# Performance work log

Measured on AMD Instinct MI355X. Metric: run time of the kernel, lower is better.

## Reference

```python
import jax, jax.numpy as jnp
import numpy as np

N = 50000
E = 800000
D_IN = 128
D_H = 128


def setup_inputs() -> dict:
    key = jax.random.key(0)
    ks = jax.random.split(key, 12)
    x = jax.random.normal(ks[0], (N, D_IN), dtype=jnp.float32)
    edge_index = jax.random.randint(ks[1], (2, E), 0, N, dtype=jnp.int32)
    reranker_scores = jax.random.uniform(ks[2], (N,), dtype=jnp.float32)
    s = 1.0 / np.sqrt(D_IN)
    # SAGEConv layer 1: lin_l (neighbors, with bias), lin_r (root, no bias)
    Wl1 = jax.random.uniform(ks[3], (D_H, D_IN), jnp.float32, -s, s)
    bl1 = jax.random.uniform(ks[4], (D_H,), jnp.float32, -s, s)
    Wr1 = jax.random.uniform(ks[5], (D_H, D_IN), jnp.float32, -s, s)
    # SAGEConv layer 2
    sh = 1.0 / np.sqrt(D_H)
    Wl2 = jax.random.uniform(ks[6], (D_H, D_H), jnp.float32, -sh, sh)
    bl2 = jax.random.uniform(ks[7], (D_H,), jnp.float32, -sh, sh)
    Wr2 = jax.random.uniform(ks[8], (D_H, D_H), jnp.float32, -sh, sh)
    # score head Linear(hidden, 1)
    Ws = jax.random.uniform(ks[9], (1, D_H), jnp.float32, -sh, sh)
    bs = jax.random.uniform(ks[10], (1,), jnp.float32, -sh, sh)
    alpha = jnp.asarray(0.65, dtype=jnp.float32)
    return {"x": x, "edge_index": edge_index, "reranker_scores": reranker_scores,
            "Wl1": Wl1, "bl1": bl1, "Wr1": Wr1,
            "Wl2": Wl2, "bl2": bl2, "Wr2": Wr2,
            "Ws": Ws, "bs": bs, "alpha": alpha}


def _sage_conv(h, src, dst, Wl, bl, Wr, n_nodes):
    # PyG SAGEConv, aggr='mean': out = lin_l(mean_j x_j) + lin_r(x_i)
    msgs = h[src]                                             # [E, d] gather
    agg = jax.ops.segment_sum(msgs, dst, num_segments=n_nodes)  # [N, d]
    cnt = jax.ops.segment_sum(jnp.ones((src.shape[0],), h.dtype), dst,
                              num_segments=n_nodes)           # [N]
    agg = agg / jnp.maximum(cnt, 1.0)[:, None]
    return agg @ Wl.T + bl + h @ Wr.T


def reference(x, edge_index, reranker_scores, Wl1, bl1, Wr1, Wl2, bl2, Wr2, Ws, bs, alpha):
    src, dst = edge_index[0], edge_index[1]
    h_in = x  # input_dim == hidden_dim -> identity residual
    h = x
    h = jax.nn.relu(_sage_conv(h, src, dst, Wl1, bl1, Wr1, N))  # dropout: eval (identity)
    h = jax.nn.relu(_sage_conv(h, src, dst, Wl2, bl2, Wr2, N))
    h = h + h_in
    gnn_scores = (h @ Ws.T + bs)[:, 0]                          # [N]
    a = jax.nn.sigmoid(alpha)
    return a * reranker_scores + (1.0 - a) * gnn_scores
```

## Files before the change

kernel.cpp:

```cpp
#include <hip/hip_runtime.h>

#define NN 50000
#define NE 800000
#define DD 128

#define NBUCK 196
#define EPB   2048
#define B1    391
#define CAP   5120
#define CONVB 12500
#define PREPB 128

typedef __attribute__((ext_vector_type(8))) short short8v;
typedef __attribute__((ext_vector_type(4))) float float4v;

static __device__ __forceinline__ unsigned short f2b(float f) {
  union { float f; unsigned u; } v; v.f = f;
  unsigned r = v.u + 0x7fff + ((v.u >> 16) & 1);
  return (unsigned short)(r >> 16);
}
static __device__ __forceinline__ float b2f(unsigned short b) {
  union { unsigned u; float f; } v; v.u = ((unsigned)b) << 16;
  return v.f;
}

static __device__ __forceinline__ void fp8w_to_bf16x4(unsigned w, short* o) {
  auto lo = __builtin_amdgcn_cvt_pk_f32_fp8(w, false);
  auto hi = __builtin_amdgcn_cvt_pk_f32_fp8(w, true);
  o[0] = (short)f2b(lo[0]); o[1] = (short)f2b(lo[1]);
  o[2] = (short)f2b(hi[0]); o[3] = (short)f2b(hi[1]);
}

static __device__ __forceinline__ int excl_scan256(int v, int* ws) {
  int t = threadIdx.x, lane = t & 63, w = t >> 6;
  int s = v;
  #pragma unroll
  for (int off = 1; off < 64; off <<= 1) {
    int u = __shfl_up(s, off);
    if (lane >= off) s += u;
  }
  if (lane == 63) ws[w] = s;
  __syncthreads();
  int add = 0;
  #pragma unroll
  for (int k = 0; k < 3; ++k)
    if (k < w) add += ws[k];
  __syncthreads();
  return add + s - v;
}


__global__ __launch_bounds__(256) void k_prep(
    const int* __restrict__ dst, int* __restrict__ ghist,
    const float* __restrict__ x, const float* __restrict__ Wsc,
    unsigned char* __restrict__ xf8, float* __restrict__ xw,
    const float* __restrict__ Wl1, const float* __restrict__ Wr1,
    const float* __restrict__ Wl2, const float* __restrict__ Wr2,
    unsigned short* __restrict__ W1, unsigned short* __restrict__ W2) {
  __shared__ int hs[NBUCK];
  const int b = blockIdx.x;
  const int t = threadIdx.x;
  if (b < B1) {
    for (int i = t; i < NBUCK; i += 256) hs[i] = 0;
    __syncthreads();
    int base = b * EPB;
    for (int i = t; i < EPB; i += 256) {
      int e = base + i;
      if (e < NE) atomicAdd(&hs[dst[e] >> 8], 1);
    }
    __syncthreads();
    for (int i = t; i < NBUCK; i += 256) ghist[b * NBUCK + i] = hs[i];
  } else if (b < B1 + CONVB) {
    int node = (b - B1) * 4 + (t >> 6);
    int lane = t & 63;
    float2 v = *(const float2*)(x + (size_t)node * DD + lane * 2);
    int p8 = __builtin_amdgcn_cvt_pk_fp8_f32(v.x, v.y, 0, false);
    *(unsigned short*)(xf8 + (size_t)node * DD + lane * 2) = (unsigned short)p8;
    float p = v.x * Wsc[lane * 2] + v.y * Wsc[lane * 2 + 1];
    #pragma unroll
    for (int m = 1; m < 64; m <<= 1) p += __shfl_xor(p, m);
    if (lane == 0) xw[node] = p;
  } else {
    int idx0 = ((b - B1 - CONVB) * 256 + t) * 2;
    #pragma unroll
    for (int u = 0; u < 2; ++u) {
      int idx = idx0 + u;
      int half = idx >> 15;
      int i = idx & 32767;
      int o = i >> 8;
      int k = i & 255;
      const float* Wl = half ? Wl2 : Wl1;
      const float* Wr = half ? Wr2 : Wr1;
      float v = (k < DD) ? Wl[o * DD + k] : Wr[o * DD + (k - DD)];
      (half ? W2 : W1)[i] = f2b(v);
    }
  }
}


__global__ __launch_bounds__(256) void scan_cols(const int* __restrict__ ghist,
                                                 int* __restrict__ goff,
                                                 int* __restrict__ btot) {
  __shared__ int ws[4];
  const int j = blockIdx.x, t = threadIdx.x;
  int b0 = 2 * t, b1 = 2 * t + 1;
  int v0 = (b0 < B1) ? ghist[b0 * NBUCK + j] : 0;
  int v1 = (b1 < B1) ? ghist[b1 * NBUCK + j] : 0;
  int excl = excl_scan256(v0 + v1, ws);
  if (b0 < B1) goff[b0 * NBUCK + j] = excl;
  if (b1 < B1) goff[b1 * NBUCK + j] = excl + v0;
  if (t == 255) btot[j] = excl + v0 + v1;
}


__global__ __launch_bounds__(256) void scatter1(const int* __restrict__ src,
                                                const int* __restrict__ dst,
                                                const int* __restrict__ goff,
                                                const int* __restrict__ btot,
                                                unsigned* __restrict__ tmp) {
  __shared__ int cur[NBUCK];
  __shared__ int ws[4];
  const int t = threadIdx.x;
  int vb = (t < NBUCK) ? btot[t] : 0;
  int exb = excl_scan256(vb, ws);
  if (t < NBUCK) cur[t] = exb + goff[blockIdx.x * NBUCK + t];
  __syncthreads();
  int base = blockIdx.x * EPB;
  for (int i = t; i < EPB; i += 256) {
    int e = base + i;
    if (e < NE) {
      int d = dst[e];
      int pos = atomicAdd(&cur[d >> 8], 1);
      tmp[pos] = ((unsigned)(d & 255) << 20) | (unsigned)src[e];
    }
  }
}


__global__ __launch_bounds__(256) void bucketsort(const unsigned* __restrict__ tmp,
                                                  const int* __restrict__ btot,
                                                  int* __restrict__ rowptr,
                                                  int* __restrict__ col) {
  __shared__ unsigned vals[CAP];
  __shared__ int cnt[256];
  __shared__ int ws[4];
  __shared__ int s0_sh;
  const int b = blockIdx.x, j = threadIdx.x;
  int vb = (j < NBUCK) ? btot[j] : 0;
  int exb = excl_scan256(vb, ws);
  if (j == b) s0_sh = exb;
  cnt[j] = 0;
  __syncthreads();
  const int s0 = s0_sh;
  int n = btot[b];
  if (n > CAP) n = CAP;
  for (int i = j; i < n; i += 256) {
    unsigned v = tmp[s0 + i];
    vals[i] = v;
    atomicAdd(&cnt[v >> 20], 1);
  }
  __syncthreads();
  int c = cnt[j];
  int excl = excl_scan256(c, ws);
  int node = b * 256 + j;
  if (node < NN) rowptr[node] = s0 + excl;
  if (b == 0 && j == 0) rowptr[NN] = NE;
  cnt[j] = excl;
  __syncthreads();
  for (int i = j; i < n; i += 256) {
    unsigned v = vals[i];
    int pos = atomicAdd(&cnt[v >> 20], 1);
    col[s0 + pos] = (int)(v & 0xFFFFF);
  }
}


__global__ __launch_bounds__(256) void agg_fp8(const unsigned char* __restrict__ hf8,
                                               const int* __restrict__ rowptr,
                                               const int* __restrict__ col,
                                               unsigned short* __restrict__ agg) {
  int node = (blockIdx.x * 256 + threadIdx.x) >> 3;
  if (node >= NN) return;
  const int q = threadIdx.x & 7;
  const unsigned char* hb = hf8 + q * 16;
  int beg = rowptr[node], end = rowptr[node + 1];
  float acc[16];
  #pragma unroll
  for (int k = 0; k < 16; ++k) acc[k] = 0.f;
  int e = beg;
  for (; e + 8 <= end; e += 8) {
    uint4 v[8];
    #pragma unroll
    for (int j = 0; j < 8; ++j)
      v[j] = *(const uint4*)(hb + (size_t)col[e + j] * DD);
    #pragma unroll
    for (int j = 0; j < 8; ++j) {
      #pragma unroll
      for (int d = 0; d < 4; ++d) {
        unsigned w = (&v[j].x)[d];
        auto lo = __builtin_amdgcn_cvt_pk_f32_fp8(w, false);
        auto hi = __builtin_amdgcn_cvt_pk_f32_fp8(w, true);
        acc[d * 4 + 0] += lo[0];
        acc[d * 4 + 1] += lo[1];
        acc[d * 4 + 2] += hi[0];
        acc[d * 4 + 3] += hi[1];
      }
    }
  }
  if (e < end) {
    uint4 v[8];
    #pragma unroll
    for (int j = 0; j < 8; ++j) {
      int idx = (e + j < end) ? (e + j) : (end - 1);
      v[j] = *(const uint4*)(hb + (size_t)col[idx] * DD);
    }
    #pragma unroll
    for (int j = 0; j < 8; ++j) {
      float m = (e + j < end) ? 1.f : 0.f;
      #pragma unroll
      for (int d = 0; d < 4; ++d) {
        unsigned w = (&v[j].x)[d];
        auto lo = __builtin_amdgcn_cvt_pk_f32_fp8(w, false);
        auto hi = __builtin_amdgcn_cvt_pk_f32_fp8(w, true);
        acc[d * 4 + 0] = fmaf(m, lo[0], acc[d * 4 + 0]);
        acc[d * 4 + 1] = fmaf(m, lo[1], acc[d * 4 + 1]);
        acc[d * 4 + 2] = fmaf(m, hi[0], acc[d * 4 + 2]);
        acc[d * 4 + 3] = fmaf(m, hi[1], acc[d * 4 + 3]);
      }
    }
  }
  float inv = 1.0f / fmaxf((float)(end - beg), 1.0f);
  short8v o0, o1;
  #pragma unroll
  for (int k = 0; k < 8; ++k) {
    o0[k] = (short)f2b(acc[k] * inv);
    o1[k] = (short)f2b(acc[8 + k] * inv);
  }
  *(short8v*)(agg + (size_t)node * DD + q * 16) = o0;
  *(short8v*)(agg + (size_t)node * DD + q * 16 + 8) = o1;
}


template <bool SCORE>
__global__ __launch_bounds__(256) void linear_mfma(
    const unsigned short* __restrict__ aggb, const unsigned char* __restrict__ hf8,
    const unsigned short* __restrict__ Wcat, const float* __restrict__ bl,
    unsigned char* __restrict__ hf8out,
    const float* __restrict__ Ws, const float* __restrict__ bsp,
    const float* __restrict__ alphap, const float* __restrict__ rr,
    const float* __restrict__ xw, float* __restrict__ out) {
  __shared__ unsigned short zl[64 * 256];
  __shared__ float sbuf[64];

  const int t = threadIdx.x;
  const int wid = t >> 6;
  const int l = t & 63;
  const int lg = l >> 4;
  const int lm = l & 15;
  const int node0 = blockIdx.x * 64;
  const int nb = wid * 32;

  short8v bfr[2][8];
  #pragma unroll
  for (int nf = 0; nf < 2; ++nf)
    #pragma unroll
    for (int kt = 0; kt < 8; ++kt)
      bfr[nf][kt] = *(const short8v*)(Wcat + (size_t)(nb + nf * 16 + lm) * 256 + kt * 32 + lg * 8);

  if (SCORE && t < 64) sbuf[t] = 0.f;

  #pragma unroll
  for (int q = 0; q < 4; ++q) {
    int idx = q * 256 + t;
    int row = idx >> 4;
    int c = idx & 15;
    int node = node0 + row; if (node >= NN) node = NN - 1;
    short8v v = *(const short8v*)(aggb + (size_t)node * DD + c * 8);
    int cs = c ^ (row & 7);
    *(short8v*)(&zl[row * 256 + cs * 8]) = v;
  }
  #pragma unroll
  for (int q = 0; q < 2; ++q) {
    int idx = q * 256 + t;
    int row = idx >> 3;
    int cp = idx & 7;
    int node = node0 + row; if (node >= NN) node = NN - 1;
    uint4 w8 = *(const uint4*)(hf8 + (size_t)node * DD + cp * 16);
    short8v v0, v1;
    fp8w_to_bf16x4(w8.x, (short*)&v0);
    fp8w_to_bf16x4(w8.y, ((short*)&v0) + 4);
    fp8w_to_bf16x4(w8.z, (short*)&v1);
    fp8w_to_bf16x4(w8.w, ((short*)&v1) + 4);
    int c0 = 16 + cp * 2;
    *(short8v*)(&zl[row * 256 + (c0 ^ (row & 7)) * 8]) = v0;
    *(short8v*)(&zl[row * 256 + ((c0 + 1) ^ (row & 7)) * 8]) = v1;
  }
  __syncthreads();

  float4v acc[4][2];
  #pragma unroll
  for (int mf = 0; mf < 4; ++mf) {
    acc[mf][0] = (float4v){0.f, 0.f, 0.f, 0.f};
    acc[mf][1] = (float4v){0.f, 0.f, 0.f, 0.f};
  }

  #pragma unroll
  for (int kt = 0; kt < 8; ++kt) {
    short8v afr[4];
    #pragma unroll
    for (int mf = 0; mf < 4; ++mf) {
      int row = mf * 16 + lm;
      int c = (kt * 4 + lg) ^ (row & 7);
      afr[mf] = *(const short8v*)(&zl[row * 256 + c * 8]);
    }
    #pragma unroll
    for (int mf = 0; mf < 4; ++mf) {
      acc[mf][0] = __builtin_amdgcn_mfma_f32_16x16x32_bf16(afr[mf], bfr[0][kt], acc[mf][0], 0, 0, 0);
      acc[mf][1] = __builtin_amdgcn_mfma_f32_16x16x32_bf16(afr[mf], bfr[1][kt], acc[mf][1], 0, 0, 0);
    }
  }

  const float b0 = bl[nb + lm];
  const float b1 = bl[nb + 16 + lm];

  if (!SCORE) {
    __syncthreads();
    #pragma unroll
    for (int mf = 0; mf < 4; ++mf) {
      #pragma unroll
      for (int r = 0; r < 4; ++r) {
        int row = mf * 16 + lg * 4 + r;
        zl[row * 256 + nb + lm]      = f2b(fmaxf(acc[mf][0][r] + b0, 0.f));
        zl[row * 256 + nb + 16 + lm] = f2b(fmaxf(acc[mf][1][r] + b1, 0.f));
      }
    }
    __syncthreads();
    #pragma unroll
    for (int i = 0; i < 2; ++i) {
      int idx = i * 256 + t;
      int row = idx >> 3;
      int c16 = idx & 7;
      int node = node0 + row;
      if (node < NN) {
        short8v v0 = *(const short8v*)(&zl[row * 256 + c16 * 16]);
        short8v v1 = *(const short8v*)(&zl[row * 256 + c16 * 16 + 8]);
        uint4 p8;
        unsigned* pw = &p8.x;
        #pragma unroll
        for (int k2 = 0; k2 < 2; ++k2) {
          const short8v& v = k2 ? v1 : v0;
          unsigned wlo = (unsigned)(unsigned short)__builtin_amdgcn_cvt_pk_fp8_f32(
              b2f((unsigned short)v[0]), b2f((unsigned short)v[1]), 0, false);
          unsigned whi = (unsigned)(unsigned short)__builtin_amdgcn_cvt_pk_fp8_f32(
              b2f((unsigned short)v[2]), b2f((unsigned short)v[3]), 0, false);
          pw[k2 * 2] = wlo | (whi << 16);
          wlo = (unsigned)(unsigned short)__builtin_amdgcn_cvt_pk_fp8_f32(
              b2f((unsigned short)v[4]), b2f((unsigned short)v[5]), 0, false);
          whi = (unsigned)(unsigned short)__builtin_amdgcn_cvt_pk_fp8_f32(
              b2f((unsigned short)v[6]), b2f((unsigned short)v[7]), 0, false);
          pw[k2 * 2 + 1] = wlo | (whi << 16);
        }
        *(uint4*)(hf8out + (size_t)node * DD + c16 * 16) = p8;
      }
    }
  } else {
    const float w0 = Ws[nb + lm];
    const float w1 = Ws[nb + 16 + lm];
    #pragma unroll
    for (int mf = 0; mf < 4; ++mf) {
      #pragma unroll
      for (int r = 0; r < 4; ++r) {
        float p = fmaxf(acc[mf][0][r] + b0, 0.f) * w0
                + fmaxf(acc[mf][1][r] + b1, 0.f) * w1;
        p += __shfl_xor(p, 1);
        p += __shfl_xor(p, 2);
        p += __shfl_xor(p, 4);
        p += __shfl_xor(p, 8);
        if (lm == 0) atomicAdd(&sbuf[mf * 16 + lg * 4 + r], p);
      }
    }
    __syncthreads();
    if (t < 64) {
      int node = node0 + t;
      if (node < NN) {
        float a = 1.f / (1.f + expf(-alphap[0]));
        float score = sbuf[t] + xw[node] + bsp[0];
        out[node] = a * rr[node] + (1.f - a) * score;
      }
    }
  }
}


extern "C" void kernel_launch(void* const* d_in, const int* in_sizes, int n_in,
                              void* d_out, int out_size, void* d_ws, size_t ws_size,
                              hipStream_t stream) {
  const float* x   = (const float*)d_in[0];
  const int*   ei  = (const int*)d_in[1];
  const float* rr  = (const float*)d_in[2];
  const float* Wl1 = (const float*)d_in[3];
  const float* bl1 = (const float*)d_in[4];
  const float* Wr1 = (const float*)d_in[5];
  const float* Wl2 = (const float*)d_in[6];
  const float* bl2 = (const float*)d_in[7];
  const float* Wr2 = (const float*)d_in[8];
  const float* Wsc = (const float*)d_in[9];
  const float* bs  = (const float*)d_in[10];
  const float* al  = (const float*)d_in[11];
  const int* srcv = ei;
  const int* dstv = ei + NE;
  float* out = (float*)d_out;

  size_t off = 0;
  auto nxt = [&](size_t bytes) {
    size_t cur = off; off += (bytes + 255) & ~(size_t)255; return cur;
  };
  int*            ghist  = (int*)((char*)d_ws + nxt((size_t)B1 * NBUCK * 4));
  int*            goff   = (int*)((char*)d_ws + nxt((size_t)B1 * NBUCK * 4));
  int*            btot   = (int*)((char*)d_ws + nxt((size_t)NBUCK * 4));
  int*            rowptr = (int*)((char*)d_ws + nxt((size_t)(NN + 1) * 4));
  int*            col    = (int*)((char*)d_ws + nxt((size_t)NE * 4));
  unsigned*       tmp    = (unsigned*)((char*)d_ws + nxt((size_t)NE * 4));
  unsigned short* aggb   = (unsigned short*)((char*)d_ws + nxt((size_t)NN * DD * 2));
  unsigned char*  xf8    = (unsigned char*)((char*)d_ws + nxt((size_t)NN * DD));
  unsigned char*  h1f8   = (unsigned char*)((char*)d_ws + nxt((size_t)NN * DD));
  unsigned short* W1     = (unsigned short*)((char*)d_ws + nxt((size_t)DD * 256 * 2));
  unsigned short* W2     = (unsigned short*)((char*)d_ws + nxt((size_t)DD * 256 * 2));
  float*          xw     = (float*)((char*)d_ws + nxt((size_t)NN * 4));

  k_prep<<<B1 + CONVB + PREPB, 256, 0, stream>>>(
      dstv, ghist, x, Wsc, xf8, xw, Wl1, Wr1, Wl2, Wr2, W1, W2);
  scan_cols<<<NBUCK, 256, 0, stream>>>(ghist, goff, btot);
  scatter1<<<B1, 256, 0, stream>>>(srcv, dstv, goff, btot, tmp);
  bucketsort<<<NBUCK, 256, 0, stream>>>(tmp, btot, rowptr, col);

  agg_fp8<<<(NN * 8 + 255) / 256, 256, 0, stream>>>(xf8, rowptr, col, aggb);
  linear_mfma<false><<<(NN + 63) / 64, 256, 0, stream>>>(
      aggb, xf8, W1, bl1, h1f8, nullptr, nullptr, nullptr, nullptr, nullptr, nullptr);
  agg_fp8<<<(NN * 8 + 255) / 256, 256, 0, stream>>>(h1f8, rowptr, col, aggb);
  linear_mfma<true><<<(NN + 63) / 64, 256, 0, stream>>>(
      aggb, h1f8, W2, bl2, nullptr, Wsc, bs, al, rr, xw, out);
}
```

Before: 104.2 us.

## Fuse histogram, scan and scatter into prep kernel via global atomic bucket slots

Replaces the three-kernel histogram/column-scan/scatter sequence with a single pass inside k_prep. Each block claims space in a fixed-capacity per-bucket region of tmp through a global atomicAdd on padded counters, then scatters its edges there. bucketsort reads each bucket's slot directly and takes the final offsets from the counters. This removes two kernel launches and the ghist/goff traffic, but adds a memset and contended global atomics. It also makes edge order within a bucket nondeterministic, and edges beyond CAP are silently dropped.

```diff
diff --git a/kernel.cpp b/kernel.cpp
--- a/kernel.cpp
+++ b/kernel.cpp
@@ -8,6 +8,7 @@
 #define EPB   2048
 #define B1    391
 #define CAP   5120
+#define GSTRIDE 64
 #define CONVB 12500
 #define PREPB 128
 
@@ -51,7 +52,8 @@
 
 
 __global__ __launch_bounds__(256) void k_prep(
-    const int* __restrict__ dst, int* __restrict__ ghist,
+    const int* __restrict__ src, const int* __restrict__ dst,
+    int* __restrict__ gcnt, unsigned* __restrict__ tmp,
     const float* __restrict__ x, const float* __restrict__ Wsc,
     unsigned char* __restrict__ xf8, float* __restrict__ xw,
     const float* __restrict__ Wl1, const float* __restrict__ Wr1,
@@ -69,7 +71,23 @@
       if (e < NE) atomicAdd(&hs[dst[e] >> 8], 1);
     }
     __syncthreads();
-    for (int i = t; i < NBUCK; i += 256) ghist[b * NBUCK + i] = hs[i];
+    for (int i = t; i < NBUCK; i += 256) {
+      int c = hs[i];
+      int st = i * CAP;
+      if (c > 0) st += atomicAdd(&gcnt[i * GSTRIDE], c);
+      hs[i] = st;
+    }
+    __syncthreads();
+    for (int i = t; i < EPB; i += 256) {
+      int e = base + i;
+      if (e < NE) {
+        int d = dst[e];
+        int j = d >> 8;
+        int pos = atomicAdd(&hs[j], 1);
+        if (pos < j * CAP + CAP)
+          tmp[pos] = ((unsigned)(d & 255) << 20) | (unsigned)src[e];
+      }
+    }
   } else if (b < B1 + CONVB) {
     int node = (b - B1) * 4 + (t >> 6);
     int lane = t & 63;
@@ -98,47 +116,8 @@
 }
 
 
-__global__ __launch_bounds__(256) void scan_cols(const int* __restrict__ ghist,
-                                                 int* __restrict__ goff,
-                                                 int* __restrict__ btot) {
-  __shared__ int ws[4];
-  const int j = blockIdx.x, t = threadIdx.x;
-  int b0 = 2 * t, b1 = 2 * t + 1;
-  int v0 = (b0 < B1) ? ghist[b0 * NBUCK + j] : 0;
-  int v1 = (b1 < B1) ? ghist[b1 * NBUCK + j] : 0;
-  int excl = excl_scan256(v0 + v1, ws);
-  if (b0 < B1) goff[b0 * NBUCK + j] = excl;
-  if (b1 < B1) goff[b1 * NBUCK + j] = excl + v0;
-  if (t == 255) btot[j] = excl + v0 + v1;
-}
-
-
-__global__ __launch_bounds__(256) void scatter1(const int* __restrict__ src,
-                                                const int* __restrict__ dst,
-                                                const int* __restrict__ goff,
-                                                const int* __restrict__ btot,
-                                                unsigned* __restrict__ tmp) {
-  __shared__ int cur[NBUCK];
-  __shared__ int ws[4];
-  const int t = threadIdx.x;
-  int vb = (t < NBUCK) ? btot[t] : 0;
-  int exb = excl_scan256(vb, ws);
-  if (t < NBUCK) cur[t] = exb + goff[blockIdx.x * NBUCK + t];
-  __syncthreads();
-  int base = blockIdx.x * EPB;
-  for (int i = t; i < EPB; i += 256) {
-    int e = base + i;
-    if (e < NE) {
-      int d = dst[e];
-      int pos = atomicAdd(&cur[d >> 8], 1);
-      tmp[pos] = ((unsigned)(d & 255) << 20) | (unsigned)src[e];
-    }
-  }
-}
-
-
 __global__ __launch_bounds__(256) void bucketsort(const unsigned* __restrict__ tmp,
-                                                  const int* __restrict__ btot,
+                                                  const int* __restrict__ gcnt,
                                                   int* __restrict__ rowptr,
                                                   int* __restrict__ col) {
   __shared__ unsigned vals[CAP];
@@ -146,16 +125,17 @@
   __shared__ int ws[4];
   __shared__ int s0_sh;
   const int b = blockIdx.x, j = threadIdx.x;
-  int vb = (j < NBUCK) ? btot[j] : 0;
+  int vb = (j < NBUCK) ? gcnt[j * GSTRIDE] : 0;
   int exb = excl_scan256(vb, ws);
   if (j == b) s0_sh = exb;
   cnt[j] = 0;
   __syncthreads();
   const int s0 = s0_sh;
-  int n = btot[b];
+  int n = gcnt[b * GSTRIDE];
   if (n > CAP) n = CAP;
+  const unsigned* tsrc = tmp + (size_t)b * CAP;
   for (int i = j; i < n; i += 256) {
-    unsigned v = tmp[s0 + i];
+    unsigned v = tsrc[i];
     vals[i] = v;
     atomicAdd(&cnt[v >> 20], 1);
   }
@@ -415,12 +395,10 @@
   auto nxt = [&](size_t bytes) {
     size_t cur = off; off += (bytes + 255) & ~(size_t)255; return cur;
   };
-  int*            ghist  = (int*)((char*)d_ws + nxt((size_t)B1 * NBUCK * 4));
-  int*            goff   = (int*)((char*)d_ws + nxt((size_t)B1 * NBUCK * 4));
-  int*            btot   = (int*)((char*)d_ws + nxt((size_t)NBUCK * 4));
+  int*            gcnt   = (int*)((char*)d_ws + nxt((size_t)NBUCK * GSTRIDE * 4));
   int*            rowptr = (int*)((char*)d_ws + nxt((size_t)(NN + 1) * 4));
   int*            col    = (int*)((char*)d_ws + nxt((size_t)NE * 4));
-  unsigned*       tmp    = (unsigned*)((char*)d_ws + nxt((size_t)NE * 4));
+  unsigned*       tmp    = (unsigned*)((char*)d_ws + nxt((size_t)NBUCK * CAP * 4));
   unsigned short* aggb   = (unsigned short*)((char*)d_ws + nxt((size_t)NN * DD * 2));
   unsigned char*  xf8    = (unsigned char*)((char*)d_ws + nxt((size_t)NN * DD));
   unsigned char*  h1f8   = (unsigned char*)((char*)d_ws + nxt((size_t)NN * DD));
@@ -428,11 +406,10 @@
   unsigned short* W2     = (unsigned short*)((char*)d_ws + nxt((size_t)DD * 256 * 2));
   float*          xw     = (float*)((char*)d_ws + nxt((size_t)NN * 4));
 
+  hipMemsetAsync(gcnt, 0, (size_t)NBUCK * GSTRIDE * 4, stream);
   k_prep<<<B1 + CONVB + PREPB, 256, 0, stream>>>(
-      dstv, ghist, x, Wsc, xf8, xw, Wl1, Wr1, Wl2, Wr2, W1, W2);
-  scan_cols<<<NBUCK, 256, 0, stream>>>(ghist, goff, btot);
-  scatter1<<<B1, 256, 0, stream>>>(srcv, dstv, goff, btot, tmp);
-  bucketsort<<<NBUCK, 256, 0, stream>>>(tmp, btot, rowptr, col);
+      srcv, dstv, gcnt, tmp, x, Wsc, xf8, xw, Wl1, Wr1, Wl2, Wr2, W1, W2);
+  bucketsort<<<NBUCK, 256, 0, stream>>>(tmp, gcnt, rowptr, col);
 
   agg_fp8<<<(NN * 8 + 255) / 256, 256, 0, stream>>>(xf8, rowptr, col, aggb);
   linear_mfma<false><<<(NN + 63) / 64, 256, 0, stream>>>(
```

Result: faster. 100.1 us (-4.0%).
